# Kernel tuning notes

Measured on AMD Instinct MI355X. Metric: run time of the kernel, lower is better.

## Reference

```python
import jax, jax.numpy as jnp
import numpy as np

B, S, D, H, HD = 4096, 50, 32, 4, 8
SCALE = 1.0 / (8 ** 0.5)


def setup_inputs() -> dict:
    key = jax.random.key(0)
    ks = jax.random.split(key, 12)
    inp = {
        'Q': jax.random.normal(ks[0], (B, S, D), dtype=jnp.float32),
        'K': jax.random.normal(ks[1], (B, S, D), dtype=jnp.float32),
        'V': jax.random.normal(ks[2], (B, S, D), dtype=jnp.float32),
        'mask': jax.random.randint(ks[3], (B, 1, S, S), 0, 2).astype(jnp.bool_),
        # Linear weights (stored as [in, out]; equivalent math to torch's x @ W.T + b)
        'WQ': jax.random.normal(ks[4], (D, D), dtype=jnp.float32) * 0.1,
        'bQ': jnp.zeros((D,), dtype=jnp.float32),
        'WK': jax.random.normal(ks[5], (D, D), dtype=jnp.float32) * 0.1,
        'bK': jnp.zeros((D,), dtype=jnp.float32),
        'WV': jax.random.normal(ks[6], (D, D), dtype=jnp.float32) * 0.1,
        'bV': jnp.zeros((D,), dtype=jnp.float32),
        'WO': jax.random.normal(ks[7], (D, D), dtype=jnp.float32) * 0.1,
        'bO': jnp.zeros((D,), dtype=jnp.float32),
    }
    return inp


def reference(Q, K, V, mask, WQ, bQ, WK, bK, WV, bV, WO, bO):
    qSrc = Q
    # fcQ/fcK/fcV are (faithfully) applied twice, as in the original forward
    q = (Q @ WQ + bQ) @ WQ + bQ
    k = (K @ WK + bK) @ WK + bK
    v = (V @ WV + bV) @ WV + bV
    # split heads: [B, S, D] -> [B, H, S, HD]
    q = q.reshape(B, S, H, HD).transpose(0, 2, 1, 3)
    k = k.reshape(B, S, H, HD).transpose(0, 2, 1, 3)
    v = v.reshape(B, S, H, HD).transpose(0, 2, 1, 3)
    score = jnp.einsum('bhqd,bhkd->bhqk', q, k) * SCALE
    score = jnp.where(mask, -jnp.inf, score)
    attn = jax.nn.softmax(score, axis=-1)
    ctx = jnp.einsum('bhqk,bhkd->bhqd', attn, v)
    ctx = ctx.transpose(0, 2, 1, 3).reshape(B, S, D)
    out = ctx @ WO + bO  # dropout is identity in eval mode
    return qSrc + out
```

## Files before the change

kernel.cpp:

```cpp
#include <hip/hip_runtime.h>

#define NB 4096
constexpr float kQscale = 0.35355339059327378f * 1.4426950408889634f;

constexpr int ST = 40;
constexpr int SV = 72;
constexpr int OFF_W  = 0;
constexpr int OFF_V2 = 0;
constexpr int OFF_A  = 5120;
constexpr int OFF_C  = 7680;
constexpr int OFF_B  = 10240;
constexpr int SH_LEN = 12800;

typedef __attribute__((ext_vector_type(8))) short bf16x8;
typedef __attribute__((ext_vector_type(4))) float f32x4;
typedef __attribute__((ext_vector_type(4))) unsigned u32x4;

__device__ __forceinline__ unsigned cvt2(float lo, float hi) {
  unsigned u;
  asm("v_cvt_pk_bf16_f32 %0, %1, %2" : "=v"(u) : "v"(lo), "v"(hi));
  return u;
}
__device__ __forceinline__ float fexp2(float x) {
  float r;
  asm("v_exp_f32 %0, %1" : "=v"(r) : "v"(x));
  return r;
}
__device__ __forceinline__ void xchF(unsigned& a, unsigned& b) {
  asm volatile("v_permlane32_swap_b32 %0, %1" : "+v"(a), "+v"(b));
  asm volatile("v_permlane16_swap_b32 %0, %1" : "+v"(a), "+v"(b));
}

__global__ __launch_bounds__(256) void mha(
    const float* __restrict__ Qg, const float* __restrict__ Kg,
    const float* __restrict__ Vg, const void* __restrict__ maskg,
    const float* __restrict__ WQg, const float* __restrict__ bQg,
    const float* __restrict__ WKg, const float* __restrict__ bKg,
    const float* __restrict__ WVg, const float* __restrict__ bVg,
    const float* __restrict__ WOg, const float* __restrict__ bOg,
    float* __restrict__ outg)
{
  __shared__ __align__(16) short SH[SH_LEN];
  __shared__ __align__(16) float sBias[128];
  __shared__ unsigned sRaw[80];

  const int t = threadIdx.x;
  const int b = blockIdx.x;
  const int lane = t & 63;
  const int wv = t >> 6;
  const int c = lane & 15, g = lane >> 4;
  const int myrow = wv*16 + c;

  auto stage_tile = [&](const float* __restrict__ src, int dstOff) {
    #pragma unroll
    for (int it = 0; it < 2; ++it) {
      const int idx = t + it*256;
      if (idx < 400) {
        const float4 x = ((const float4*)src)[idx];
        const int s = idx >> 3, qd = idx & 7;
        *(uint2*)&SH[dstOff + s*ST + qd*4] = make_uint2(cvt2(x.x, x.y), cvt2(x.z, x.w));
      }
    }
  };

  auto projStep = [&](bf16x8 xb, int wm, int biasOff, int yOff, float scale) {
    #pragma unroll
    for (int Ni = 0; Ni < 2; ++Ni) {
      const bf16x8 wa = *(const bf16x8*)&SH[OFF_W + wm*1280 + (Ni*16 + c)*ST + g*8];
      const float4 bv = *(const float4*)&sBias[biasOff + Ni*16 + g*4];
      f32x4 acc = {bv.x, bv.y, bv.z, bv.w};
      acc = __builtin_amdgcn_mfma_f32_16x16x32_bf16(wa, xb, acc, 0, 0, 0);
      *(uint2*)&SH[yOff + myrow*ST + Ni*16 + g*4] =
          make_uint2(cvt2(acc[0]*scale, acc[1]*scale), cvt2(acc[2]*scale, acc[3]*scale));
    }
  };

  const unsigned w64det = ((const unsigned*)maskg)[lane];
  unsigned valB[10];
  #pragma unroll
  for (int cc = 0; cc < 10; ++cc) {
    const int idx = (wv*10 + cc)*64 + lane;
    valB[cc] = (idx < 2500) ? (unsigned)((const unsigned char*)maskg)[b*2500 + idx] : 0u;
  }
  stage_tile(Kg + b*1600, OFF_A);
  stage_tile(Qg + b*1600, OFF_C);
  stage_tile(Vg + b*1600, OFF_B);
  {
    const int wd = t & 31, wk0 = (t >> 5) * 4;
    #pragma unroll
    for (int m = 0; m < 4; ++m) {
      const float* Wp = (m == 0) ? WQg : (m == 1) ? WKg : (m == 2) ? WVg : WOg;
      const float w0 = Wp[(wk0+0)*32 + wd];
      const float w1 = Wp[(wk0+1)*32 + wd];
      const float w2 = Wp[(wk0+2)*32 + wd];
      const float w3 = Wp[(wk0+3)*32 + wd];
      *(uint2*)&SH[OFF_W + m*1280 + wd*ST + wk0] = make_uint2(cvt2(w0,w1), cvt2(w2,w3));
    }
  }
  if      (t < 32)  sBias[t] = bQg[t];
  else if (t < 64)  sBias[t] = bKg[t-32];
  else if (t < 96)  sBias[t] = bVg[t-64];
  else if (t < 128) sBias[t] = bOg[t-96];
  {
    const bool byteMask = (__ballot(w64det > 1u) != 0ull);
    #pragma unroll
    for (int cc = 0; cc < 10; ++cc) {
      const int ch = wv*10 + cc;
      const int idx = ch*64 + lane;
      unsigned val;
      if (byteMask) val = valB[cc];
      else          val = (idx < 2500) ? ((const unsigned*)maskg)[b*2500 + idx] : 0u;
      const unsigned long long m = __ballot(val != 0u);
      if (lane == 0) {
        sRaw[ch*2]     = (unsigned)m;
        sRaw[ch*2 + 1] = (unsigned)(m >> 32);
      }
    }
  }
  __syncthreads();

  {
    const bf16x8 aK = *(const bf16x8*)&SH[OFF_A + myrow*ST + g*8];
    const bf16x8 aV = *(const bf16x8*)&SH[OFF_B + myrow*ST + g*8];
    const bf16x8 aQ = *(const bf16x8*)&SH[OFF_C + myrow*ST + g*8];
    projStep(aK, 1, 32, OFF_A, 1.f);
    projStep(aV, 2, 64, OFF_B, 1.f);
    projStep(aQ, 0, 0,  OFF_C, 1.f);
  }
  f32x4 vacc0, vacc1;
  {
    const bf16x8 aK = *(const bf16x8*)&SH[OFF_A + myrow*ST + g*8];
    const bf16x8 aV = *(const bf16x8*)&SH[OFF_B + myrow*ST + g*8];
    const bf16x8 aQ = *(const bf16x8*)&SH[OFF_C + myrow*ST + g*8];
    projStep(aK, 1, 32, OFF_A, 1.f);
    projStep(aQ, 0, 0, OFF_C, kQscale);
    const bf16x8 b0 = *(const bf16x8*)&SH[OFF_W + 2*1280 + c*ST + g*8];
    const bf16x8 b1 = *(const bf16x8*)&SH[OFF_W + 2*1280 + (16 + c)*ST + g*8];
    const float bv0 = sBias[64 + c], bv1 = sBias[64 + 16 + c];
    f32x4 z0 = {bv0, bv0, bv0, bv0}, z1 = {bv1, bv1, bv1, bv1};
    vacc0 = __builtin_amdgcn_mfma_f32_16x16x32_bf16(aV, b0, z0, 0, 0, 0);
    vacc1 = __builtin_amdgcn_mfma_f32_16x16x32_bf16(aV, b1, z1, 0, 0, 0);
  }
  __syncthreads();

  {
    const int j0 = wv*16 + g*4;
    const float v0 = (j0+0 < 50) ? vacc0[0] : 0.f;
    const float v1 = (j0+1 < 50) ? vacc0[1] : 0.f;
    const float v2 = (j0+2 < 50) ? vacc0[2] : 0.f;
    const float v3 = (j0+3 < 50) ? vacc0[3] : 0.f;
    *(uint2*)&SH[OFF_V2 + c*SV + j0] = make_uint2(cvt2(v0,v1), cvt2(v2,v3));
    const float u0 = (j0+0 < 50) ? vacc1[0] : 0.f;
    const float u1 = (j0+1 < 50) ? vacc1[1] : 0.f;
    const float u2 = (j0+2 < 50) ? vacc1[2] : 0.f;
    const float u3 = (j0+3 < 50) ? vacc1[3] : 0.f;
    *(uint2*)&SH[OFF_V2 + (16 + c)*SV + j0] = make_uint2(cvt2(u0,u1), cvt2(u2,u3));
  }
  unsigned mm0, mm1;
  {
    const int bp = (myrow < 50) ? 50*myrow : 0;
    const unsigned ra = sRaw[(bp >> 5) + 0];
    const unsigned rb = sRaw[(bp >> 5) + 1];
    const unsigned rc = sRaw[(bp >> 5) + 2];
    const unsigned sh = bp & 31;
    mm0 = (unsigned)((((unsigned long long)rb << 32) | ra) >> sh);
    mm1 = (unsigned)((((unsigned long long)rc << 32) | rb) >> sh);
    if (myrow >= 50) { mm0 = ~0u; mm1 = ~0u; }
  }
  const bf16x8 qb = *(const bf16x8*)&SH[OFF_C + myrow*ST + g*8];
  bf16x8 kf[4];
  #pragma unroll
  for (int Ni = 0; Ni < 4; ++Ni)
    kf[Ni] = *(const bf16x8*)&SH[OFF_A + (Ni*16 + c)*ST + g*8];
  __syncthreads();

  const bf16x8 zf = {0,0,0,0,0,0,0,0};
  unsigned ox0[4], ox1[4];
  #pragma unroll
  for (int h = 0; h < 4; ++h) {
    const bf16x8 vf0 = *(const bf16x8*)&SH[OFF_V2 + (h*8 + (c & 7))*SV + g*8];
    const bf16x8 vf1 = *(const bf16x8*)&SH[OFF_V2 + (h*8 + (c & 7))*SV + 32 + g*8];
    const bf16x8 qh = (g == h) ? qb : zf;
    unsigned pk[8];
    float rs = 0.f;
    #pragma unroll
    for (int Ni = 0; Ni < 4; ++Ni) {
      f32x4 z = {0.f, 0.f, 0.f, 0.f};
      const f32x4 s = __builtin_amdgcn_mfma_f32_16x16x32_bf16(kf[Ni], qh, z, 0, 0, 0);
      const unsigned w = (Ni < 2) ? mm0 : mm1;
      float p[4];
      #pragma unroll
      for (int r = 0; r < 4; ++r) {
        const int key = Ni*16 + g*4 + r;
        const bool keep = (key < 50) && (((w >> (key & 31)) & 1u) == 0u);
        p[r] = keep ? fexp2(s[r]) : 0.f;
        rs += p[r];
      }
      pk[Ni*2]   = cvt2(p[0], p[1]);
      pk[Ni*2+1] = cvt2(p[2], p[3]);
    }
    rs += __shfl_xor(rs, 16);
    rs += __shfl_xor(rs, 32);
    const float ri = __builtin_amdgcn_rcpf(rs);
    unsigned w0 = pk[0], w2 = pk[2];  xchF(w0, w2);
    unsigned w1 = pk[1], w3 = pk[3];  xchF(w1, w3);
    unsigned x0 = pk[4], x2 = pk[6];  xchF(x0, x2);
    unsigned x1 = pk[5], x3 = pk[7];  xchF(x1, x3);
    const u32x4 w0v = {w0, w1, w2, w3};
    const u32x4 w1v = {x0, x1, x2, x3};
    const bf16x8 pf0 = __builtin_bit_cast(bf16x8, w0v);
    const bf16x8 pf1 = __builtin_bit_cast(bf16x8, w1v);
    f32x4 cac = {0.f, 0.f, 0.f, 0.f};
    cac = __builtin_amdgcn_mfma_f32_16x16x32_bf16(vf0, pf0, cac, 0, 0, 0);
    cac = __builtin_amdgcn_mfma_f32_16x16x32_bf16(vf1, pf1, cac, 0, 0, 0);
    ox0[h] = cvt2(cac[0]*ri, cac[1]*ri);
    ox1[h] = cvt2(cac[2]*ri, cac[3]*ri);
  }

  {
    float res[2][4];
    #pragma unroll
    for (int Nj = 0; Nj < 2; ++Nj)
      #pragma unroll
      for (int r = 0; r < 4; ++r) {
        const int row = wv*16 + g*4 + r;
        res[Nj][r] = (row < 50) ? Qg[b*1600 + row*32 + Nj*16 + c] : 0.f;
      }
    unsigned a0 = ox0[0], a1 = ox0[1], a2 = ox0[2], a3 = ox0[3];
    xchF(a0, a1);
    xchF(a2, a3);
    xchF(a0, a2);
    xchF(a1, a3);
    unsigned c0 = ox1[0], c1 = ox1[1], c2 = ox1[2], c3 = ox1[3];
    xchF(c0, c1);
    xchF(c2, c3);
    xchF(c0, c2);
    xchF(c1, c3);
    const u32x4 afv = {a0, c0, a1, c1};
    const bf16x8 af = __builtin_bit_cast(bf16x8, afv);
    #pragma unroll
    for (int Nj = 0; Nj < 2; ++Nj) {
      const bf16x8 bbf = *(const bf16x8*)&SH[OFF_W + 3*1280 + (Nj*16 + c)*ST + g*8];
      const float bv = sBias[96 + Nj*16 + c];
      f32x4 o = {bv, bv, bv, bv};
      o = __builtin_amdgcn_mfma_f32_16x16x32_bf16(af, bbf, o, 0, 0, 0);
      #pragma unroll
      for (int r = 0; r < 4; ++r) {
        const int row = wv*16 + g*4 + r;
        if (row < 50)
          outg[b*1600 + row*32 + Nj*16 + c] = o[r] + res[Nj][r];
      }
    }
  }
}

extern "C" void kernel_launch(void* const* d_in, const int* in_sizes, int n_in,
                              void* d_out, int out_size, void* d_ws, size_t ws_size,
                              hipStream_t stream) {
  const float* Q  = (const float*)d_in[0];
  const float* K  = (const float*)d_in[1];
  const float* V  = (const float*)d_in[2];
  const void*  M  = d_in[3];
  const float* WQ = (const float*)d_in[4];
  const float* bQ = (const float*)d_in[5];
  const float* WK = (const float*)d_in[6];
  const float* bK = (const float*)d_in[7];
  const float* WV = (const float*)d_in[8];
  const float* bV = (const float*)d_in[9];
  const float* WO = (const float*)d_in[10];
  const float* bO = (const float*)d_in[11];
  float* out = (float*)d_out;
  (void)d_ws; (void)ws_size; (void)in_sizes; (void)n_in; (void)out_size;

  hipLaunchKernelGGL(mha, dim3(NB), dim3(256), 0, stream,
                     Q, K, V, M, WQ, bQ, WK, bK, WV, bV, WO, bO, out);
}
```

Baseline: 56.46 us.

## Keep projection intermediates in registers via lane permutes instead of LDS round-trips

Q/K/V rows are now loaded straight from global memory into MFMA fragment registers instead of being staged through shared memory. The first projection's outputs are rearranged into the next MFMA's input layout with permlane swaps, so they are not written to LDS and read back. Only the final K projection goes to LDS, for cross-wave access, which shrinks shared memory use and removes LDS traffic and stores. The cost is more register pressure and uncoalesced 32-byte per-lane global loads.

```diff
diff --git a/kernel.cpp b/kernel.cpp
--- a/kernel.cpp
+++ b/kernel.cpp
@@ -7,10 +7,8 @@
 constexpr int SV = 72;
 constexpr int OFF_W  = 0;
 constexpr int OFF_V2 = 0;
-constexpr int OFF_A  = 5120;
-constexpr int OFF_C  = 7680;
-constexpr int OFF_B  = 10240;
-constexpr int SH_LEN = 12800;
+constexpr int OFF_K2 = 5120;
+constexpr int SH_LEN = 7680;
 
 typedef __attribute__((ext_vector_type(8))) short bf16x8;
 typedef __attribute__((ext_vector_type(4))) float f32x4;
@@ -51,29 +49,22 @@
   const int c = lane & 15, g = lane >> 4;
   const int myrow = wv*16 + c;
 
-  auto stage_tile = [&](const float* __restrict__ src, int dstOff) {
-    #pragma unroll
-    for (int it = 0; it < 2; ++it) {
-      const int idx = t + it*256;
-      if (idx < 400) {
-        const float4 x = ((const float4*)src)[idx];
-        const int s = idx >> 3, qd = idx & 7;
-        *(uint2*)&SH[dstOff + s*ST + qd*4] = make_uint2(cvt2(x.x, x.y), cvt2(x.z, x.w));
-      }
-    }
+  auto mkfrag = [&](float4 x0, float4 x1) -> bf16x8 {
+    const u32x4 u = {cvt2(x0.x,x0.y), cvt2(x0.z,x0.w), cvt2(x1.x,x1.y), cvt2(x1.z,x1.w)};
+    return __builtin_bit_cast(bf16x8, u);
   };
 
-  auto projStep = [&](bf16x8 xb, int wm, int biasOff, int yOff, float scale) {
-    #pragma unroll
-    for (int Ni = 0; Ni < 2; ++Ni) {
-      const bf16x8 wa = *(const bf16x8*)&SH[OFF_W + wm*1280 + (Ni*16 + c)*ST + g*8];
-      const float4 bv = *(const float4*)&sBias[biasOff + Ni*16 + g*4];
-      f32x4 acc = {bv.x, bv.y, bv.z, bv.w};
-      acc = __builtin_amdgcn_mfma_f32_16x16x32_bf16(wa, xb, acc, 0, 0, 0);
-      *(uint2*)&SH[yOff + myrow*ST + Ni*16 + g*4] =
-          make_uint2(cvt2(acc[0]*scale, acc[1]*scale), cvt2(acc[2]*scale, acc[3]*scale));
-    }
-  };
+  bf16x8 xbK, xbQ, xbV;
+  {
+    const int ra = b*1600 + ((myrow < 50) ? myrow : 0)*32 + g*8;
+    const float4 ka = *(const float4*)&Kg[ra];
+    const float4 kb = *(const float4*)&Kg[ra + 4];
+    const float4 qa = *(const float4*)&Qg[ra];
+    const float4 qc = *(const float4*)&Qg[ra + 4];
+    const float4 va = *(const float4*)&Vg[ra];
+    const float4 vb = *(const float4*)&Vg[ra + 4];
+    xbK = mkfrag(ka, kb); xbQ = mkfrag(qa, qc); xbV = mkfrag(va, vb);
+  }
 
   const unsigned w64det = ((const unsigned*)maskg)[lane];
   unsigned valB[10];
@@ -82,9 +73,6 @@
     const int idx = (wv*10 + cc)*64 + lane;
     valB[cc] = (idx < 2500) ? (unsigned)((const unsigned char*)maskg)[b*2500 + idx] : 0u;
   }
-  stage_tile(Kg + b*1600, OFF_A);
-  stage_tile(Qg + b*1600, OFF_C);
-  stage_tile(Vg + b*1600, OFF_B);
   {
     const int wd = t & 31, wk0 = (t >> 5) * 4;
     #pragma unroll
@@ -119,27 +107,57 @@
   }
   __syncthreads();
 
-  {
-    const bf16x8 aK = *(const bf16x8*)&SH[OFF_A + myrow*ST + g*8];
-    const bf16x8 aV = *(const bf16x8*)&SH[OFF_B + myrow*ST + g*8];
-    const bf16x8 aQ = *(const bf16x8*)&SH[OFF_C + myrow*ST + g*8];
-    projStep(aK, 1, 32, OFF_A, 1.f);
-    projStep(aV, 2, 64, OFF_B, 1.f);
-    projStep(aQ, 0, 0,  OFF_C, 1.f);
-  }
+  unsigned mm0, mm1;
+  {
+    const int bp = (myrow < 50) ? 50*myrow : 0;
+    const unsigned ra = sRaw[(bp >> 5) + 0];
+    const unsigned rb = sRaw[(bp >> 5) + 1];
+    const unsigned rc = sRaw[(bp >> 5) + 2];
+    const unsigned sh = bp & 31;
+    mm0 = (unsigned)((((unsigned long long)rb << 32) | ra) >> sh);
+    mm1 = (unsigned)((((unsigned long long)rc << 32) | rb) >> sh);
+    if (myrow >= 50) { mm0 = ~0u; mm1 = ~0u; }
+  }
+
+  auto projR = [&](bf16x8 xb, int wm, int biasOff, float scale) -> bf16x8 {
+    const bf16x8 wa0 = *(const bf16x8*)&SH[OFF_W + wm*1280 + c*ST + g*8];
+    const bf16x8 wa1 = *(const bf16x8*)&SH[OFF_W + wm*1280 + (16 + c)*ST + g*8];
+    const float4 bv0 = *(const float4*)&sBias[biasOff + g*4];
+    const float4 bv1 = *(const float4*)&sBias[biasOff + 16 + g*4];
+    f32x4 c0 = {bv0.x, bv0.y, bv0.z, bv0.w};
+    f32x4 c1 = {bv1.x, bv1.y, bv1.z, bv1.w};
+    c0 = __builtin_amdgcn_mfma_f32_16x16x32_bf16(wa0, xb, c0, 0, 0, 0);
+    c1 = __builtin_amdgcn_mfma_f32_16x16x32_bf16(wa1, xb, c1, 0, 0, 0);
+    unsigned A0 = cvt2(c0[0]*scale, c0[1]*scale), A1 = cvt2(c0[2]*scale, c0[3]*scale);
+    unsigned B0 = cvt2(c1[0]*scale, c1[1]*scale), B1 = cvt2(c1[2]*scale, c1[3]*scale);
+    xchF(A0, B0); xchF(A1, B1);
+    const u32x4 u = {A0, A1, B0, B1};
+    return __builtin_bit_cast(bf16x8, u);
+  };
+
+  const bf16x8 k1f = projR(xbK, 1, 32, 1.f);
+  const bf16x8 v1f = projR(xbV, 2, 64, 1.f);
+  const bf16x8 q1f = projR(xbQ, 0, 0,  1.f);
+  {
+    #pragma unroll
+    for (int Ni = 0; Ni < 2; ++Ni) {
+      const bf16x8 wa = *(const bf16x8*)&SH[OFF_W + 1*1280 + (Ni*16 + c)*ST + g*8];
+      const float4 bv = *(const float4*)&sBias[32 + Ni*16 + g*4];
+      f32x4 acc = {bv.x, bv.y, bv.z, bv.w};
+      acc = __builtin_amdgcn_mfma_f32_16x16x32_bf16(wa, k1f, acc, 0, 0, 0);
+      *(uint2*)&SH[OFF_K2 + myrow*ST + Ni*16 + g*4] =
+          make_uint2(cvt2(acc[0], acc[1]), cvt2(acc[2], acc[3]));
+    }
+  }
+  const bf16x8 qb = projR(q1f, 0, 0, kQscale);
   f32x4 vacc0, vacc1;
   {
-    const bf16x8 aK = *(const bf16x8*)&SH[OFF_A + myrow*ST + g*8];
-    const bf16x8 aV = *(const bf16x8*)&SH[OFF_B + myrow*ST + g*8];
-    const bf16x8 aQ = *(const bf16x8*)&SH[OFF_C + myrow*ST + g*8];
-    projStep(aK, 1, 32, OFF_A, 1.f);
-    projStep(aQ, 0, 0, OFF_C, kQscale);
-    const bf16x8 b0 = *(const bf16x8*)&SH[OFF_W + 2*1280 + c*ST + g*8];
-    const bf16x8 b1 = *(const bf16x8*)&SH[OFF_W + 2*1280 + (16 + c)*ST + g*8];
+    const bf16x8 wb0 = *(const bf16x8*)&SH[OFF_W + 2*1280 + c*ST + g*8];
+    const bf16x8 wb1 = *(const bf16x8*)&SH[OFF_W + 2*1280 + (16 + c)*ST + g*8];
     const float bv0 = sBias[64 + c], bv1 = sBias[64 + 16 + c];
     f32x4 z0 = {bv0, bv0, bv0, bv0}, z1 = {bv1, bv1, bv1, bv1};
-    vacc0 = __builtin_amdgcn_mfma_f32_16x16x32_bf16(aV, b0, z0, 0, 0, 0);
-    vacc1 = __builtin_amdgcn_mfma_f32_16x16x32_bf16(aV, b1, z1, 0, 0, 0);
+    vacc0 = __builtin_amdgcn_mfma_f32_16x16x32_bf16(v1f, wb0, z0, 0, 0, 0);
+    vacc1 = __builtin_amdgcn_mfma_f32_16x16x32_bf16(v1f, wb1, z1, 0, 0, 0);
   }
   __syncthreads();
 
@@ -156,22 +174,10 @@
     const float u3 = (j0+3 < 50) ? vacc1[3] : 0.f;
     *(uint2*)&SH[OFF_V2 + (16 + c)*SV + j0] = make_uint2(cvt2(u0,u1), cvt2(u2,u3));
   }
-  unsigned mm0, mm1;
-  {
-    const int bp = (myrow < 50) ? 50*myrow : 0;
-    const unsigned ra = sRaw[(bp >> 5) + 0];
-    const unsigned rb = sRaw[(bp >> 5) + 1];
-    const unsigned rc = sRaw[(bp >> 5) + 2];
-    const unsigned sh = bp & 31;
-    mm0 = (unsigned)((((unsigned long long)rb << 32) | ra) >> sh);
-    mm1 = (unsigned)((((unsigned long long)rc << 32) | rb) >> sh);
-    if (myrow >= 50) { mm0 = ~0u; mm1 = ~0u; }
-  }
-  const bf16x8 qb = *(const bf16x8*)&SH[OFF_C + myrow*ST + g*8];
   bf16x8 kf[4];
   #pragma unroll
   for (int Ni = 0; Ni < 4; ++Ni)
-    kf[Ni] = *(const bf16x8*)&SH[OFF_A + (Ni*16 + c)*ST + g*8];
+    kf[Ni] = *(const bf16x8*)&SH[OFF_K2 + (Ni*16 + c)*ST + g*8];
   __syncthreads();
 
   const bf16x8 zf = {0,0,0,0,0,0,0,0};
```

Result: faster. 54.62 us (-3.3%).
